# Performance work log

Hardware: AMD Instinct MI355X
Metric: run time of the kernel (lower is better)

## Reference

```python
import jax, jax.numpy as jnp
import numpy as np

D_MODEL, D_STATE, D_CONV, EXPAND = 1024, 16, 4, 2
D_INNER = D_MODEL * EXPAND


def setup_inputs() -> dict:
    key = jax.random.key(0)
    ks = jax.random.split(key, 12)
    s = lambda fan_in: 1.0 / np.sqrt(fan_in)
    return {
        "x": jax.random.normal(ks[0], (2, 2048, D_MODEL), dtype=jnp.float32),
        "W_in": jax.random.normal(ks[1], (D_MODEL, 2 * D_INNER), dtype=jnp.float32) * s(D_MODEL),
        "b_in": jnp.zeros((2 * D_INNER,), jnp.float32),
        "W_conv": jax.random.normal(ks[2], (D_INNER, 1, D_CONV), dtype=jnp.float32) * s(D_CONV),
        "b_conv": jnp.zeros((D_INNER,), jnp.float32),
        "A_log": jax.random.normal(ks[3], (D_INNER, D_STATE), dtype=jnp.float32) * -0.5 - 1.0,
        "D": jnp.ones((D_INNER,), jnp.float32),
        "W_B": jax.random.normal(ks[4], (D_INNER, D_STATE), dtype=jnp.float32) * s(D_INNER),
        "b_B": jnp.zeros((D_STATE,), jnp.float32),
        "W_C": jax.random.normal(ks[5], (D_INNER, D_STATE), dtype=jnp.float32) * s(D_INNER),
        "b_C": jnp.zeros((D_STATE,), jnp.float32),
        "W_out": jax.random.normal(ks[6], (D_INNER, D_MODEL), dtype=jnp.float32) * s(D_INNER),
        "b_out": jnp.zeros((D_MODEL,), jnp.float32),
    }


def reference(x, W_in, b_in, W_conv, b_conv, A_log, D, W_B, b_B, W_C, b_C, W_out, b_out):
    B, L, _ = x.shape
    xz = x @ W_in + b_in                       # (B, L, 2*D_INNER)
    xi, z = jnp.split(xz, 2, axis=-1)
    # depthwise causal conv1d (left pad d_conv-1, truncate to L)
    xc = jnp.swapaxes(xi, 1, 2)                # (B, D_INNER, L)
    xc = jax.lax.conv_general_dilated(
        xc, W_conv, window_strides=(1,), padding=[(D_CONV - 1, 0)],
        dimension_numbers=("NCH", "OIH", "NCH"), feature_group_count=D_INNER)
    xc = xc + b_conv[None, :, None]
    xi = jnp.swapaxes(xc, 1, 2)                # (B, L, D_INNER)
    xi = jax.nn.silu(xi)

    A = -jnp.exp(jnp.clip(A_log, -10.0, 2.0))  # (D_INNER, D_STATE)
    Bm = xi @ W_B + b_B                        # (B, L, D_STATE)
    Cm = xi @ W_C + b_C                        # (B, L, D_STATE)

    def step(h, inp):
        x_t, B_t, C_t = inp                    # (B,D_INNER), (B,D_STATE), (B,D_STATE)
        h = h * A[None] + x_t[:, :, None] * B_t[:, None, :]
        h = jnp.clip(h, -100.0, 100.0)
        y = jnp.einsum("bds,bs->bd", h, C_t) + D * x_t
        y = jnp.clip(y, -100.0, 100.0)
        return h, y

    h0 = jnp.zeros((B, D_INNER, D_STATE), x.dtype)
    xs = (jnp.swapaxes(xi, 0, 1), jnp.swapaxes(Bm, 0, 1), jnp.swapaxes(Cm, 0, 1))
    _, ys = jax.lax.scan(step, h0, xs)         # ys: (L, B, D_INNER)
    y = jnp.swapaxes(ys, 0, 1)                 # (B, L, D_INNER)
    y = y * jax.nn.sigmoid(z)
    return y @ W_out + b_out
```

## Files before the change

kernel.cpp:

```cpp
#include <hip/hip_runtime.h>
#include <hip/hip_bf16.h>
#include <math.h>

#define B_SZ   2
#define L_SZ   2048
#define DM     1024
#define DI     2048
#define DS     16
#define M_SZ   (B_SZ * L_SZ)
#define N_XZ   (2 * DI)
#define LDF    20
#define SEGS   32
#define SEGLEN 64
#define SEG1   32

typedef short bf16x8 __attribute__((ext_vector_type(8)));
typedef float f32x4  __attribute__((ext_vector_type(4)));

__device__ __forceinline__ unsigned short rne16(float f) {
  unsigned int u = __builtin_bit_cast(unsigned int, f);
  u += 0x7FFFu + ((u >> 16) & 1u);
  return (unsigned short)(u >> 16);
}
__device__ __forceinline__ float frombf(unsigned short h) {
  unsigned int u = ((unsigned int)h) << 16;
  return __builtin_bit_cast(float, u);
}

__global__ __launch_bounds__(256) void convert_x(
    const float* __restrict__ x, unsigned short* __restrict__ xh,
    unsigned short* __restrict__ xl) {
  int i = (blockIdx.x * 256 + threadIdx.x) * 4;
  float4 v = *(const float4*)(x + i);
  unsigned short h0 = rne16(v.x), h1 = rne16(v.y), h2 = rne16(v.z), h3 = rne16(v.w);
  *(ushort4*)(xh + i) = make_ushort4(h0, h1, h2, h3);
  *(ushort4*)(xl + i) = make_ushort4(rne16(v.x - frombf(h0)), rne16(v.y - frombf(h1)),
                                     rne16(v.z - frombf(h2)), rne16(v.w - frombf(h3)));
}

__global__ __launch_bounds__(256) void transpose_w(
    const float* __restrict__ in, int R, int C,
    unsigned short* __restrict__ oh, unsigned short* __restrict__ ol) {
  __shared__ float T[64][65];
  const int tid = threadIdx.x;
  const int c0 = blockIdx.x * 64, r0 = blockIdx.y * 64;
  const int cc = tid & 63, rq = tid >> 6;
  #pragma unroll
  for (int i = 0; i < 16; ++i) {
    int r = rq * 16 + i;
    T[r][cc] = in[(size_t)(r0 + r) * C + c0 + cc];
  }
  __syncthreads();
  #pragma unroll
  for (int i = 0; i < 16; ++i) {
    int c = rq * 16 + i;
    float v = T[cc][c];
    size_t o = (size_t)(c0 + c) * R + r0 + cc;
    unsigned short h = rne16(v);
    oh[o] = h;
    if (ol) ol[o] = rne16(v - frombf(h));
  }
}

template<int BN, bool X3, bool OUTBF16>
__global__ __launch_bounds__(256, X3 ? 3 : 4) void gemm_t(
    const unsigned short* __restrict__ Ah, const unsigned short* __restrict__ Al, int lda,
    const unsigned short* __restrict__ Bh, const unsigned short* __restrict__ Bl, int ldb,
    const float* __restrict__ bias, float* __restrict__ Cf,
    unsigned short* __restrict__ Cz, int ldc, int K) {
  constexpr int WN  = BN / 2;
  constexpr int FJ  = BN / 32;
  constexpr int BCH = BN / 64;
  __shared__ unsigned int AhS[128 * LDF];
  __shared__ unsigned int BhS[BN * LDF];
  __shared__ unsigned int AlS[X3 ? 128 * LDF : 4];
  __shared__ unsigned int BlS[X3 ? BN * LDF : 4];
  const int tid  = threadIdx.x;
  const int lane = tid & 63, wave = tid >> 6;
  const int wr = wave >> 1, wc = wave & 1;
  const int lm = lane & 15, lq = lane >> 4;
  const int row0 = blockIdx.y * 128, col0 = blockIdx.x * BN;

  f32x4 acc[4][FJ];
  #pragma unroll
  for (int i = 0; i < 4; ++i)
    #pragma unroll
    for (int j = 0; j < FJ; ++j) acc[i][j] = (f32x4){0.f, 0.f, 0.f, 0.f};

  for (int k0 = 0; k0 < K; k0 += 32) {
    __syncthreads();
    #pragma unroll
    for (int i = 0; i < 2; ++i) {
      int idx = tid + i * 256, r = idx >> 2, q = idx & 3;
      size_t go = (size_t)(row0 + r) * lda + k0 + q * 8;
      *(uint4*)&AhS[r * LDF + q * 4] = *(const uint4*)(Ah + go);
      if constexpr (X3)
        *(uint4*)&AlS[r * LDF + q * 4] = *(const uint4*)(Al + go);
    }
    #pragma unroll
    for (int i = 0; i < BCH; ++i) {
      int idx = tid + i * 256, r = idx >> 2, q = idx & 3;
      size_t go = (size_t)(col0 + r) * ldb + k0 + q * 8;
      *(uint4*)&BhS[r * LDF + q * 4] = *(const uint4*)(Bh + go);
      if constexpr (X3)
        *(uint4*)&BlS[r * LDF + q * 4] = *(const uint4*)(Bl + go);
    }
    __syncthreads();
    bf16x8 bh[FJ], bl[FJ];
    #pragma unroll
    for (int j = 0; j < FJ; ++j) {
      bh[j] = *(const bf16x8*)&BhS[(wc * WN + j * 16 + lm) * LDF + lq * 4];
      if constexpr (X3)
        bl[j] = *(const bf16x8*)&BlS[(wc * WN + j * 16 + lm) * LDF + lq * 4];
    }
    #pragma unroll
    for (int i = 0; i < 4; ++i) {
      bf16x8 ah = *(const bf16x8*)&AhS[(wr * 64 + i * 16 + lm) * LDF + lq * 4];
      bf16x8 al;
      if constexpr (X3)
        al = *(const bf16x8*)&AlS[(wr * 64 + i * 16 + lm) * LDF + lq * 4];
      #pragma unroll
      for (int j = 0; j < FJ; ++j) {
        acc[i][j] = __builtin_amdgcn_mfma_f32_16x16x32_bf16(ah, bh[j], acc[i][j], 0, 0, 0);
        if constexpr (X3) {
          acc[i][j] = __builtin_amdgcn_mfma_f32_16x16x32_bf16(ah, bl[j], acc[i][j], 0, 0, 0);
          acc[i][j] = __builtin_amdgcn_mfma_f32_16x16x32_bf16(al, bh[j], acc[i][j], 0, 0, 0);
        }
      }
    }
  }
  #pragma unroll
  for (int i = 0; i < 4; ++i) {
    #pragma unroll
    for (int j = 0; j < FJ; ++j) {
      int c = col0 + wc * WN + j * 16 + lm;
      float bs = bias[c];
      #pragma unroll
      for (int k = 0; k < 4; ++k) {
        int r = row0 + wr * 64 + i * 16 + lq * 4 + k;
        float v = acc[i][j][k] + bs;
        if constexpr (OUTBF16) Cz[(size_t)r * ldc + c] = rne16(v);
        else                   Cf[(size_t)r * ldc + c] = v;
      }
    }
  }
}

__global__ __launch_bounds__(256) void conv_silu_kernel(
    const float* __restrict__ xi, const float* __restrict__ Wc,
    const float* __restrict__ bc, float* __restrict__ xc) {
  int idx = blockIdx.x * blockDim.x + threadIdx.x;
  if (idx >= M_SZ * DI) return;
  int d  = idx & (DI - 1);
  int bl = idx >> 11;
  int l  = bl & (L_SZ - 1);
  float4 w = ((const float4*)Wc)[d];
  const float* base = xi + (size_t)bl * DI + d;
  float s = bc[d] + base[0] * w.w;
  if (l >= 1) s = fmaf(base[-DI],     w.z, s);
  if (l >= 2) s = fmaf(base[-2 * DI], w.y, s);
  if (l >= 3) s = fmaf(base[-3 * DI], w.x, s);
  float sig = 1.f / (1.f + expf(-s));
  xc[idx] = s * sig;
}

__global__ __launch_bounds__(256) void gemm_bc_kernel(
    const float* __restrict__ xc,
    const float* __restrict__ WB, const float* __restrict__ bB,
    const float* __restrict__ WC, const float* __restrict__ bC,
    float* __restrict__ BCm, float* __restrict__ Bp2) {
  int t = blockIdx.x * blockDim.x + threadIdx.x;
  int row = t >> 5;
  int cc  = t & 31;
  int s   = cc & 15;
  const float* W = (cc < 16) ? WB : WC;
  const float4* xr4 = (const float4*)(xc + (size_t)row * DI);
  float acc = 0.f;
  #pragma unroll 4
  for (int k4 = 0; k4 < DI / 4; ++k4) {
    float4 xv = xr4[k4];
    int k = k4 * 4;
    acc = fmaf(xv.x, W[(k    ) * DS + s], acc);
    acc = fmaf(xv.y, W[(k + 1) * DS + s], acc);
    acc = fmaf(xv.z, W[(k + 2) * DS + s], acc);
    acc = fmaf(xv.w, W[(k + 3) * DS + s], acc);
  }
  if (cc < 16) {
    float v = acc + bB[s];
    BCm[row * 32 + s * 2] = v;
    Bp2[(size_t)(row >> 1) * 32 + s * 2 + (row & 1)] = v;
  } else {
    BCm[row * 32 + s * 2 + 1] = acc + bC[s];
  }
}


__device__ __forceinline__ float clampA(float a) {
  return fminf(fmaxf(a, -10.f), 2.f);
}

__global__ __launch_bounds__(256, 1) void scan_pass1(
    const float* __restrict__ xc, const float* __restrict__ Bp2,
    const float* __restrict__ A_log, float* __restrict__ hseg) {
  const int b    = blockIdx.y;
  const int wave = threadIdx.x >> 6;
  const int lane = threadIdx.x & 63;
  const int dd   = lane >> 4, s = lane & 15;
  const int d    = blockIdx.x * 16 + wave * 4 + dd;

  const float A = -expf(clampA(A_log[d * DS + s]));
  float h = 0.f;

  const float* px = xc  + (size_t)b * L_SZ * DI + d;
  const float* pb = Bp2 + (size_t)b * (L_SZ / 2) * 32 + s * 2;

  float  x0[SEG1], x1[SEG1];
  float2 b0[SEG1 / 2], b1[SEG1 / 2];

  #pragma unroll
  for (int j = 0; j < SEG1; ++j) x0[j] = px[j * DI];
  #pragma unroll
  for (int j = 0; j < SEG1 / 2; ++j) b0[j] = *(const float2*)(pb + j * 32);
  px += SEG1 * DI; pb += (SEG1 / 2) * 32;

  for (int w = 0; w < 60; w += 2) {
    #pragma unroll
    for (int j = 0; j < SEG1; ++j) x1[j] = px[j * DI];
    #pragma unroll
    for (int j = 0; j < SEG1 / 2; ++j) b1[j] = *(const float2*)(pb + j * 32);
    px += SEG1 * DI; pb += (SEG1 / 2) * 32;
    #pragma unroll
    for (int j = 0; j < SEG1; ++j) {
      float bj = (j & 1) ? b0[j >> 1].y : b0[j >> 1].x;
      h = __builtin_amdgcn_fmed3f(fmaf(h, A, x0[j] * bj), -100.f, 100.f);
    }
    #pragma unroll
    for (int j = 0; j < SEG1; ++j) x0[j] = px[j * DI];
    #pragma unroll
    for (int j = 0; j < SEG1 / 2; ++j) b0[j] = *(const float2*)(pb + j * 32);
    px += SEG1 * DI; pb += (SEG1 / 2) * 32;
    #pragma unroll
    for (int j = 0; j < SEG1; ++j) {
      float bj = (j & 1) ? b1[j >> 1].y : b1[j >> 1].x;
      h = __builtin_amdgcn_fmed3f(fmaf(h, A, x1[j] * bj), -100.f, 100.f);
    }
    hseg[(((size_t)b * (SEGS - 1) + (w >> 1)) * DI + d) * DS + s] = h;
  }
  #pragma unroll
  for (int j = 0; j < SEG1; ++j) x1[j] = px[j * DI];
  #pragma unroll
  for (int j = 0; j < SEG1 / 2; ++j) b1[j] = *(const float2*)(pb + j * 32);
  #pragma unroll
  for (int j = 0; j < SEG1; ++j) {
    float bj = (j & 1) ? b0[j >> 1].y : b0[j >> 1].x;
    h = __builtin_amdgcn_fmed3f(fmaf(h, A, x0[j] * bj), -100.f, 100.f);
  }
  #pragma unroll
  for (int j = 0; j < SEG1; ++j) {
    float bj = (j & 1) ? b1[j >> 1].y : b1[j >> 1].x;
    h = __builtin_amdgcn_fmed3f(fmaf(h, A, x1[j] * bj), -100.f, 100.f);
  }
  hseg[(((size_t)b * (SEGS - 1) + 30) * DI + d) * DS + s] = h;
}

__global__ __launch_bounds__(256, 2) void scan_pass2(
    const float* __restrict__ xc, const float* __restrict__ BCm,
    const unsigned short* __restrict__ zb,
    const float* __restrict__ A_log, const float* __restrict__ Dv,
    const float* __restrict__ hseg, unsigned short* __restrict__ yg) {
  const int b   = blockIdx.y >> 5;
  const int seg = blockIdx.y & 31;
  const int d   = blockIdx.x * 256 + threadIdx.x;

  float A[16], h[16];
  #pragma unroll
  for (int q = 0; q < 4; ++q) {
    float4 al = *(const float4*)(A_log + d * DS + q * 4);
    A[q * 4 + 0] = -expf(clampA(al.x));
    A[q * 4 + 1] = -expf(clampA(al.y));
    A[q * 4 + 2] = -expf(clampA(al.z));
    A[q * 4 + 3] = -expf(clampA(al.w));
  }
  const float Dr = Dv[d];
  if (seg == 0) {
    #pragma unroll
    for (int s = 0; s < 16; ++s) h[s] = 0.f;
  } else {
    const float* hp = hseg + (((size_t)b * (SEGS - 1) + seg - 1) * DI + d) * DS;
    #pragma unroll
    for (int q = 0; q < 4; ++q) {
      float4 hv = *(const float4*)(hp + q * 4);
      h[q * 4 + 0] = hv.x; h[q * 4 + 1] = hv.y;
      h[q * 4 + 2] = hv.z; h[q * 4 + 3] = hv.w;
    }
  }

  const int rbase = b * L_SZ + seg * SEGLEN;
  const float*          px  = xc  + (size_t)rbase * DI + d;
  const unsigned short* pz  = zb  + (size_t)rbase * DI + d;
  unsigned short*       py  = yg  + (size_t)rbase * DI + d;
  const float*          pbc = BCm + (size_t)rbase * 32;

  #pragma unroll 2
  for (int t = 0; t < SEGLEN; ++t) {
    const float x = px[t * DI];
    const float* bc = pbc + t * 32;
    float y = Dr * x;
    #pragma unroll
    for (int s = 0; s < 16; ++s) {
      h[s] = __builtin_amdgcn_fmed3f(fmaf(h[s], A[s], x * bc[s * 2]), -100.f, 100.f);
      y = fmaf(h[s], bc[s * 2 + 1], y);
    }
    y = __builtin_amdgcn_fmed3f(y, -100.f, 100.f);
    const float zf = frombf(pz[t * DI]);
    py[t * DI] = rne16(y * (1.f / (1.f + expf(-zf))));
  }
}

extern "C" void kernel_launch(void* const* d_in, const int* in_sizes, int n_in,
                              void* d_out, int out_size, void* d_ws, size_t ws_size,
                              hipStream_t stream) {
  const float* x      = (const float*)d_in[0];
  const float* W_in   = (const float*)d_in[1];
  const float* b_in   = (const float*)d_in[2];
  const float* W_conv = (const float*)d_in[3];
  const float* b_conv = (const float*)d_in[4];
  const float* A_log  = (const float*)d_in[5];
  const float* Dv     = (const float*)d_in[6];
  const float* W_B    = (const float*)d_in[7];
  const float* b_B    = (const float*)d_in[8];
  const float* W_C    = (const float*)d_in[9];
  const float* b_C    = (const float*)d_in[10];
  const float* W_out  = (const float*)d_in[11];
  const float* b_out  = (const float*)d_in[12];
  float* out = (float*)d_out;

  char* w = (char*)d_ws;
  float*          xi   = (float*)(w + 0);
  unsigned short* yg   = (unsigned short*)(w + 0);
  float*          hseg = (float*)(w + 16777216);
  float*          BCm  = (float*)(w + 25165824);
  float*          Bp2  = (float*)(w + 25690112);
  unsigned short* zb   = (unsigned short*)(w + 33554432);
  float*          xc   = (float*)(w + 50331648);
  unsigned short* xh   = (unsigned short*)(w + 50331648);
  unsigned short* xl   = (unsigned short*)(w + 58720256);
  unsigned short* WhT  = (unsigned short*)(w + 67108864);
  unsigned short* WlT  = (unsigned short*)(w + 75497472);
  unsigned short* WoT  = (unsigned short*)(w + 84410368);

  convert_x<<<M_SZ * DM / 1024, 256, 0, stream>>>(x, xh, xl);
  transpose_w<<<dim3(N_XZ / 64, DM / 64), 256, 0, stream>>>(W_in, DM, N_XZ, WhT, WlT);
  transpose_w<<<dim3(DM / 64, DI / 64), 256, 0, stream>>>(W_out, DI, DM, WoT, nullptr);

  gemm_t<128, true, false><<<dim3(DI / 128, M_SZ / 128), 256, 0, stream>>>(
      xh, xl, DM, WhT, WlT, DM, b_in, xi, nullptr, DI, DM);

  gemm_t<128, false, true><<<dim3(DI / 128, M_SZ / 128), 256, 0, stream>>>(
      xh, nullptr, DM, WhT + (size_t)DI * DM, nullptr, DM,
      b_in + DI, nullptr, zb, DI, DM);

  conv_silu_kernel<<<M_SZ * DI / 256, 256, 0, stream>>>(xi, W_conv, b_conv, xc);

  gemm_bc_kernel<<<M_SZ * 32 / 256, 256, 0, stream>>>(xc, W_B, b_B, W_C, b_C, BCm, Bp2);

  scan_pass1<<<dim3(DI / 16, B_SZ), 256, 0, stream>>>(xc, Bp2, A_log, hseg);

  scan_pass2<<<dim3(DI / 256, B_SZ * SEGS), 256, 0, stream>>>(
      xc, BCm, zb, A_log, Dv, hseg, yg);

  gemm_t<64, false, false><<<dim3(DM / 64, M_SZ / 128), 256, 0, stream>>>(
      yg, nullptr, DI, WoT, nullptr, DI, b_out, out, nullptr, DM, DI);
}
```

Measured before the change: 428.4 us.

## Compute B/C projection with split-K bf16x3 MFMA GEMM plus reduction

```diff
diff --git a/kernel.cpp b/kernel.cpp
--- a/kernel.cpp
+++ b/kernel.cpp
@@ -13,6 +13,7 @@
 #define SEGS   32
 #define SEGLEN 64
 #define SEG1   32
+#define KZN    8
 
 typedef short bf16x8 __attribute__((ext_vector_type(8)));
 typedef float f32x4  __attribute__((ext_vector_type(4)));
@@ -164,36 +165,111 @@
   xc[idx] = s * sig;
 }
 
-__global__ __launch_bounds__(256) void gemm_bc_kernel(
-    const float* __restrict__ xc,
-    const float* __restrict__ WB, const float* __restrict__ bB,
-    const float* __restrict__ WC, const float* __restrict__ bC,
-    float* __restrict__ BCm, float* __restrict__ Bp2) {
-  int t = blockIdx.x * blockDim.x + threadIdx.x;
-  int row = t >> 5;
-  int cc  = t & 31;
-  int s   = cc & 15;
-  const float* W = (cc < 16) ? WB : WC;
-  const float4* xr4 = (const float4*)(xc + (size_t)row * DI);
-  float acc = 0.f;
-  #pragma unroll 4
-  for (int k4 = 0; k4 < DI / 4; ++k4) {
-    float4 xv = xr4[k4];
-    int k = k4 * 4;
-    acc = fmaf(xv.x, W[(k    ) * DS + s], acc);
-    acc = fmaf(xv.y, W[(k + 1) * DS + s], acc);
-    acc = fmaf(xv.z, W[(k + 2) * DS + s], acc);
-    acc = fmaf(xv.w, W[(k + 3) * DS + s], acc);
-  }
-  if (cc < 16) {
-    float v = acc + bB[s];
-    BCm[row * 32 + s * 2] = v;
-    Bp2[(size_t)(row >> 1) * 32 + s * 2 + (row & 1)] = v;
-  } else {
-    BCm[row * 32 + s * 2 + 1] = acc + bC[s];
-  }
-}
-
+__global__ __launch_bounds__(256) void prep_wbc(
+    const float* __restrict__ WB, const float* __restrict__ WC,
+    unsigned short* __restrict__ Wh, unsigned short* __restrict__ Wl) {
+  int idx = blockIdx.x * 256 + threadIdx.x;
+  int c = idx >> 11, k = idx & 2047;
+  float v = 0.f;
+  if (c < 32) {
+    const float* W = (c & 1) ? WC : WB;
+    v = W[k * DS + (c >> 1)];
+  }
+  unsigned short h = rne16(v);
+  Wh[idx] = h;
+  Wl[idx] = rne16(v - frombf(h));
+}
+
+__global__ __launch_bounds__(256, 3) void gemm_bcf(
+    const float* __restrict__ Af, int lda,
+    const unsigned short* __restrict__ Bh, const unsigned short* __restrict__ Bl, int ldb,
+    float* __restrict__ parts, int ldc, int Kslice) {
+  __shared__ unsigned int AhS[128 * LDF];
+  __shared__ unsigned int AlS[128 * LDF];
+  __shared__ unsigned int BhS[64 * LDF];
+  __shared__ unsigned int BlS[64 * LDF];
+  const int tid  = threadIdx.x;
+  const int lane = tid & 63, wave = tid >> 6;
+  const int wr = wave >> 1, wc = wave & 1;
+  const int lm = lane & 15, lq = lane >> 4;
+  const int row0 = blockIdx.y * 128;
+  const int kbase = blockIdx.x * Kslice;
+  float* Cp = parts + (size_t)blockIdx.x * M_SZ * 64;
+
+  f32x4 acc[4][2];
+  #pragma unroll
+  for (int i = 0; i < 4; ++i)
+    #pragma unroll
+    for (int j = 0; j < 2; ++j) acc[i][j] = (f32x4){0.f, 0.f, 0.f, 0.f};
+
+  for (int k0 = kbase; k0 < kbase + Kslice; k0 += 32) {
+    __syncthreads();
+    #pragma unroll
+    for (int i = 0; i < 4; ++i) {
+      int idx = tid + i * 256, r = idx >> 3, q = idx & 7;
+      float4 v = *(const float4*)(Af + (size_t)(row0 + r) * lda + k0 + q * 4);
+      unsigned short h0 = rne16(v.x), h1 = rne16(v.y), h2 = rne16(v.z), h3 = rne16(v.w);
+      AhS[r * LDF + q * 2]     = (unsigned)h0 | ((unsigned)h1 << 16);
+      AhS[r * LDF + q * 2 + 1] = (unsigned)h2 | ((unsigned)h3 << 16);
+      unsigned short l0 = rne16(v.x - frombf(h0)), l1 = rne16(v.y - frombf(h1));
+      unsigned short l2 = rne16(v.z - frombf(h2)), l3 = rne16(v.w - frombf(h3));
+      AlS[r * LDF + q * 2]     = (unsigned)l0 | ((unsigned)l1 << 16);
+      AlS[r * LDF + q * 2 + 1] = (unsigned)l2 | ((unsigned)l3 << 16);
+    }
+    {
+      int r = tid >> 2, q = tid & 3;
+      size_t go = (size_t)r * ldb + k0 + q * 8;
+      *(uint4*)&BhS[r * LDF + q * 4] = *(const uint4*)(Bh + go);
+      *(uint4*)&BlS[r * LDF + q * 4] = *(const uint4*)(Bl + go);
+    }
+    __syncthreads();
+    bf16x8 bh[2], bl[2];
+    #pragma unroll
+    for (int j = 0; j < 2; ++j) {
+      bh[j] = *(const bf16x8*)&BhS[(wc * 32 + j * 16 + lm) * LDF + lq * 4];
+      bl[j] = *(const bf16x8*)&BlS[(wc * 32 + j * 16 + lm) * LDF + lq * 4];
+    }
+    #pragma unroll
+    for (int i = 0; i < 4; ++i) {
+      bf16x8 ah = *(const bf16x8*)&AhS[(wr * 64 + i * 16 + lm) * LDF + lq * 4];
+      bf16x8 al = *(const bf16x8*)&AlS[(wr * 64 + i * 16 + lm) * LDF + lq * 4];
+      #pragma unroll
+      for (int j = 0; j < 2; ++j) {
+        acc[i][j] = __builtin_amdgcn_mfma_f32_16x16x32_bf16(ah, bh[j], acc[i][j], 0, 0, 0);
+        acc[i][j] = __builtin_amdgcn_mfma_f32_16x16x32_bf16(ah, bl[j], acc[i][j], 0, 0, 0);
+        acc[i][j] = __builtin_amdgcn_mfma_f32_16x16x32_bf16(al, bh[j], acc[i][j], 0, 0, 0);
+      }
+    }
+  }
+  #pragma unroll
+  for (int i = 0; i < 4; ++i) {
+    #pragma unroll
+    for (int j = 0; j < 2; ++j) {
+      int c = wc * 32 + j * 16 + lm;
+      #pragma unroll
+      for (int k = 0; k < 4; ++k) {
+        int r = row0 + wr * 64 + i * 16 + lq * 4 + k;
+        Cp[(size_t)r * ldc + c] = acc[i][j][k];
+      }
+    }
+  }
+}
+
+__global__ __launch_bounds__(256) void prep_bc_sum(
+    const float* __restrict__ parts,
+    const float* __restrict__ bB, const float* __restrict__ bC,
+    float* __restrict__ BCm2, float* __restrict__ Bp2) {
+  int idx = blockIdx.x * 256 + threadIdx.x;
+  int row = idx >> 5, c = idx & 31;
+  float s = 0.f;
+  #pragma unroll
+  for (int kz = 0; kz < KZN; ++kz)
+    s += parts[(size_t)kz * M_SZ * 64 + (size_t)row * 64 + c];
+  s += (c & 1) ? bC[c >> 1] : bB[c >> 1];
+  BCm2[(size_t)row * 64 + c] = s;
+  if (!(c & 1))
+    Bp2[(size_t)(row >> 1) * 32 + (c >> 1) * 2 + (row & 1)] = s;
+}
 
 __device__ __forceinline__ float clampA(float a) {
   return fminf(fmaxf(a, -10.f), 2.f);
@@ -264,7 +340,7 @@
 }
 
 __global__ __launch_bounds__(256, 2) void scan_pass2(
-    const float* __restrict__ xc, const float* __restrict__ BCm,
+    const float* __restrict__ xc, const float* __restrict__ BCm2,
     const unsigned short* __restrict__ zb,
     const float* __restrict__ A_log, const float* __restrict__ Dv,
     const float* __restrict__ hseg, unsigned short* __restrict__ yg) {
@@ -299,12 +375,12 @@
   const float*          px  = xc  + (size_t)rbase * DI + d;
   const unsigned short* pz  = zb  + (size_t)rbase * DI + d;
   unsigned short*       py  = yg  + (size_t)rbase * DI + d;
-  const float*          pbc = BCm + (size_t)rbase * 32;
+  const float*          pbc = BCm2 + (size_t)rbase * 64;
 
   #pragma unroll 2
   for (int t = 0; t < SEGLEN; ++t) {
     const float x = px[t * DI];
-    const float* bc = pbc + t * 32;
+    const float* bc = pbc + t * 64;
     float y = Dr * x;
     #pragma unroll
     for (int s = 0; s < 16; ++s) {
@@ -336,22 +412,26 @@
   float* out = (float*)d_out;
 
   char* w = (char*)d_ws;
-  float*          xi   = (float*)(w + 0);
-  unsigned short* yg   = (unsigned short*)(w + 0);
-  float*          hseg = (float*)(w + 16777216);
-  float*          BCm  = (float*)(w + 25165824);
-  float*          Bp2  = (float*)(w + 25690112);
-  unsigned short* zb   = (unsigned short*)(w + 33554432);
-  float*          xc   = (float*)(w + 50331648);
-  unsigned short* xh   = (unsigned short*)(w + 50331648);
-  unsigned short* xl   = (unsigned short*)(w + 58720256);
-  unsigned short* WhT  = (unsigned short*)(w + 67108864);
-  unsigned short* WlT  = (unsigned short*)(w + 75497472);
-  unsigned short* WoT  = (unsigned short*)(w + 84410368);
+  float*          xi    = (float*)(w + 0);
+  unsigned short* yg    = (unsigned short*)(w + 0);
+  float*          parts = (float*)(w + 16777216);
+  float*          hseg  = (float*)(w + 16777216);
+  float*          BCm2  = (float*)(w + 25165824);
+  float*          Bp2   = (float*)(w + 26214400);
+  unsigned short* zb    = (unsigned short*)(w + 33554432);
+  float*          xc    = (float*)(w + 50331648);
+  unsigned short* xh    = (unsigned short*)(w + 50331648);
+  unsigned short* xl    = (unsigned short*)(w + 58720256);
+  unsigned short* WhT   = (unsigned short*)(w + 67108864);
+  unsigned short* WlT   = (unsigned short*)(w + 75497472);
+  unsigned short* WbcTh = (unsigned short*)(w + 83886080);
+  unsigned short* WbcTl = (unsigned short*)(w + 84148224);
+  unsigned short* WoT   = (unsigned short*)(w + 84410368);
 
   convert_x<<<M_SZ * DM / 1024, 256, 0, stream>>>(x, xh, xl);
   transpose_w<<<dim3(N_XZ / 64, DM / 64), 256, 0, stream>>>(W_in, DM, N_XZ, WhT, WlT);
   transpose_w<<<dim3(DM / 64, DI / 64), 256, 0, stream>>>(W_out, DI, DM, WoT, nullptr);
+  prep_wbc<<<64 * 2048 / 256, 256, 0, stream>>>(W_B, W_C, WbcTh, WbcTl);
 
   gemm_t<128, true, false><<<dim3(DI / 128, M_SZ / 128), 256, 0, stream>>>(
       xh, xl, DM, WhT, WlT, DM, b_in, xi, nullptr, DI, DM);
@@ -362,12 +442,14 @@
 
   conv_silu_kernel<<<M_SZ * DI / 256, 256, 0, stream>>>(xi, W_conv, b_conv, xc);
 
-  gemm_bc_kernel<<<M_SZ * 32 / 256, 256, 0, stream>>>(xc, W_B, b_B, W_C, b_C, BCm, Bp2);
+  gemm_bcf<<<dim3(KZN, M_SZ / 128), 256, 0, stream>>>(
+      xc, DI, WbcTh, WbcTl, DI, parts, 64, DI / KZN);
+  prep_bc_sum<<<M_SZ * 32 / 256, 256, 0, stream>>>(parts, b_B, b_C, BCm2, Bp2);
 
   scan_pass1<<<dim3(DI / 16, B_SZ), 256, 0, stream>>>(xc, Bp2, A_log, hseg);
 
   scan_pass2<<<dim3(DI / 256, B_SZ * SEGS), 256, 0, stream>>>(
-      xc, BCm, zb, A_log, Dv, hseg, yg);
+      xc, BCm2, zb, A_log, Dv, hseg, yg);
 
   gemm_t<64, false, false><<<dim3(DM / 64, M_SZ / 128), 256, 0, stream>>>(
       yg, nullptr, DI, WoT, nullptr, DI, b_out, out, nullptr, DM, DI);
```

Measured after the change: 393.1 us. 8.3% less time.
